# Performance work log

Hardware: AMD Instinct MI355X
Metric: run time of the kernel (lower is better)

## Reference

```python
import jax, jax.numpy as jnp
import numpy as np

N_HEAD, N_KV, HEAD_DIM, GATE_CH = 16, 4, 128, 32

def _rope(x, cos, sin):
    d = x.shape[3] // 2
    x1, x2 = x[..., :d], x[..., d:]
    return jnp.concatenate([x1 * cos + x2 * sin, x1 * (-sin) + x2 * cos], axis=3)

def _rmsnorm(x):
    xf = x.astype(jnp.float32)
    return (x * jax.lax.rsqrt(jnp.mean(xf * xf, axis=-1, keepdims=True) + 1e-6)).astype(x.dtype)

def setup_inputs() -> dict:
    key = jax.random.key(0)
    ks = jax.random.split(key, 9)
    B, T, C = 2, 2048, 2048
    return {
        "x":  jax.random.normal(ks[0], (B, T, C), jnp.float32),
        "ve": jax.random.normal(ks[1], (B, T, N_KV * HEAD_DIM), jnp.float32),
        "cos": jax.random.uniform(ks[2], (T, 1, HEAD_DIM // 2), jnp.float32),
        "sin": jax.random.uniform(ks[3], (T, 1, HEAD_DIM // 2), jnp.float32),
        "Wq": jax.random.normal(ks[4], (C, N_HEAD * HEAD_DIM), jnp.float32) * 0.02,
        "Wk": jax.random.normal(ks[5], (C, N_KV * HEAD_DIM), jnp.float32) * 0.02,
        "Wv": jax.random.normal(ks[6], (C, N_KV * HEAD_DIM), jnp.float32) * 0.02,
        "Wg": jax.random.normal(ks[7], (GATE_CH, N_KV), jnp.float32) * 0.02,
        "Wo": jax.random.normal(ks[8], (C, C), jnp.float32) * 0.02,
        "window": 1024,
    }

def reference(x, ve, cos, sin, Wq, Wk, Wv, Wg, Wo, window):
    B, T, C = x.shape
    q = (x @ Wq).reshape(B, T, N_HEAD, HEAD_DIM)
    k = (x @ Wk).reshape(B, T, N_KV, HEAD_DIM)
    v = (x @ Wv).reshape(B, T, N_KV, HEAD_DIM)
    # value-embedding gate (ve_gate active for this layer)
    gate = 2.0 * jax.nn.sigmoid(x[..., :GATE_CH] @ Wg)  # (B,T,N_KV)
    v = v + gate[..., None] * ve.reshape(B, T, N_KV, HEAD_DIM)
    q, k = _rope(q, cos, sin), _rope(k, cos, sin)
    q, k = _rmsnorm(q), _rmsnorm(k)
    # GQA: repeat kv heads (repeat_interleave over head dim)
    groups = N_HEAD // N_KV
    k = jnp.repeat(k, groups, axis=2)
    v = jnp.repeat(v, groups, axis=2)
    scale = 1.0 / np.sqrt(HEAD_DIM)
    scores = jnp.einsum("bthd,bshd->bhts", q, k) * scale  # (B,H,T,T)
    idx = jnp.arange(T)
    diff = idx[None, :] - idx[:, None]  # diff[i,j] = j - i, as in torch code
    mask = (diff >= 0) & (diff < window)
    scores = jnp.where(mask[None, None], scores, -jnp.inf)
    p = jax.nn.softmax(scores, axis=-1)
    y = jnp.einsum("bhts,bshd->bthd", p, v).reshape(B, T, C)
    return y @ Wo
```

## Files before the change

kernel.cpp:

```cpp
#include <hip/hip_runtime.h>
#include <hip/hip_bf16.h>
#include <cstdint>

typedef __hip_bfloat16 bf16;
typedef __attribute__((ext_vector_type(8))) short short8;
typedef __attribute__((ext_vector_type(4))) short short4v;
typedef __attribute__((ext_vector_type(4))) float f32x4;

#define T_   2048
#define CDIM 2048
#define NH   16
#define NKV  4
#define HD   128
#define QSCALE (0.08838834764831845f * 1.44269504088896340f)

__device__ __forceinline__ void gload_lds16(const void* g, void* l) {
  __builtin_amdgcn_global_load_lds(
      (const __attribute__((address_space(1))) void*)g,
      (__attribute__((address_space(3))) void*)l, 16, 0, 0);
}

template <int G> __device__ __forceinline__ void vm_gate() {
  if constexpr (G == 6)      asm volatile("s_waitcnt vmcnt(6)" ::: "memory");
  else if constexpr (G == 5) asm volatile("s_waitcnt vmcnt(5)" ::: "memory");
  else                       asm volatile("s_waitcnt vmcnt(0)" ::: "memory");
}

__global__ __launch_bounds__(256) void cast_x_kernel(const float4* __restrict__ in,
                                                     ushort4* __restrict__ out, int n4) {
  int i = blockIdx.x * 256 + threadIdx.x;
  if (i >= n4) return;
  float4 v = in[i];
  union { bf16 h[4]; ushort4 u; } cv;
  cv.h[0] = __float2bfloat16(v.x);
  cv.h[1] = __float2bfloat16(v.y);
  cv.h[2] = __float2bfloat16(v.z);
  cv.h[3] = __float2bfloat16(v.w);
  out[i] = cv.u;
}

__global__ __launch_bounds__(256) void cast_transpose(const float* __restrict__ W,
                                                      bf16* __restrict__ WT,
                                                      int K, int N) {
  __shared__ float tile[32][33];
  int k0 = blockIdx.y * 32, n0 = blockIdx.x * 32;
  int r = threadIdx.x >> 5, c = threadIdx.x & 31;
  for (int i = 0; i < 4; ++i)
    tile[r + i * 8][c] = W[(size_t)(k0 + r + i * 8) * N + n0 + c];
  __syncthreads();
  for (int i = 0; i < 4; ++i)
    WT[(size_t)(n0 + r + i * 8) * K + k0 + c] = __float2bfloat16(tile[c][r + i * 8]);
}

template <int MREP, int NREP, typename CT>
__global__ __launch_bounds__(512, 2) void gemm_pp(const bf16* __restrict__ A,
                                                  const bf16* __restrict__ BT,
                                                  CT* __restrict__ C,
                                                  int N, int K, int RY, int RX) {
  constexpr int BM = MREP * 32;
  constexpr int BN = NREP * 64;
  constexpr int QN = (MREP == 8) ? 4 : 2;
  constexpr int MI = MREP / 4;
  constexpr int GATE = NREP + QN - 1;
  __shared__ __align__(16) bf16 sA[2][BM * 64];
  __shared__ __align__(16) bf16 sB[2][BN * 64];

  int tid = threadIdx.x;
  int lane = tid & 63, w = tid >> 6;
  int wm = w >> 2, wn = w & 3;
  int lr = lane & 15, lk = lane >> 4;

  int xcd = blockIdx.x & 7, t = blockIdx.x >> 3;
  int by = (xcd >> 1) * RY + t / RX;
  int bx = (xcd & 1) * RX + t % RX;
  int m0 = by * BM, n0 = bx * BN;

  f32x4 acc[MREP][NREP];
#pragma unroll
  for (int m = 0; m < MREP; ++m)
#pragma unroll
    for (int n = 0; n < NREP; ++n) acc[m][n] = (f32x4){0.f, 0.f, 0.f, 0.f};

  const bf16* Abase = A + (size_t)m0 * K;
  const bf16* Bbase = BT + (size_t)n0 * K;

  auto stageB = [&](int p, int kt) {
    int kb = kt << 6;
#pragma unroll
    for (int i = 0; i < NREP; ++i) {
      int c = i * 512 + tid;
      int r = c >> 3, sl = c & 7;
      gload_lds16(Bbase + (size_t)r * K + kb + ((sl ^ (r & 7)) << 3),
                  (char*)(&sB[p][0]) + c * 16);
    }
  };
  auto stageAq = [&](int p, int kt, int q) {
    int kb = kt << 6;
    int rbase = 32 * q + ((w & 3) << 3) + ((w >> 2) * (BM / 2));
    int r = rbase + (lane >> 3), sl = lane & 7;
    gload_lds16(Abase + (size_t)r * K + kb + ((sl ^ (r & 7)) << 3),
                (char*)(&sA[p][0]) + rbase * 128 + lane * 16);
  };

  int nk = K >> 6;
  stageB(0, 0);
#pragma unroll
  for (int q = 0; q < QN; ++q) stageAq(0, 0, q);
  stageB(1, 1);
#pragma unroll
  for (int q = 0; q < QN - 1; ++q) stageAq(1, 1, q);
  vm_gate<GATE>();
  __builtin_amdgcn_s_barrier();

#define READ_A_FRAGS(PH)                                                   \
  {                                                                        \
    _Pragma("unroll")                                                      \
    for (int mi = 0; mi < MI; ++mi) {                                      \
      int row = wm * (MREP * 16) + ((PH) * MI + mi) * 16 + lr;             \
      const char* rb = sAb + row * 128;                                    \
      int rx = (row & 7) << 4;                                             \
      af[mi][0] = *(const short8*)(rb + ((lk * 16) ^ rx));                 \
      af[mi][1] = *(const short8*)(rb + ((64 + lk * 16) ^ rx));            \
    }                                                                      \
  }
#define MFMA_PH(PH)                                                        \
  __builtin_amdgcn_s_setprio(1);                                           \
  _Pragma("unroll")                                                        \
  for (int kk = 0; kk < 2; ++kk)                                           \
    _Pragma("unroll")                                                      \
    for (int mi = 0; mi < MI; ++mi)                                        \
      _Pragma("unroll")                                                    \
      for (int n = 0; n < NREP; ++n)                                       \
        acc[(PH) * MI + mi][n] = __builtin_amdgcn_mfma_f32_16x16x32_bf16(  \
            af[mi][kk], bfr[n][kk], acc[(PH) * MI + mi][n], 0, 0, 0);      \
  __builtin_amdgcn_s_setprio(0);
#define LGKM_FENCE                                                         \
  asm volatile("s_waitcnt lgkmcnt(0)" ::: "memory");                       \
  __builtin_amdgcn_sched_barrier(0);

  for (int kt = 0; kt < nk; ++kt) {
    int p = kt & 1;
    const char* sAb = (const char*)(&sA[p][0]);
    const char* sBb = (const char*)(&sB[p][0]);
    short8 bfr[NREP][2], af[MI][2];

#pragma unroll
    for (int n = 0; n < NREP; ++n) {
      int row = wn * (NREP * 16) + n * 16 + lr;
      const char* rb = sBb + row * 128;
      int rx = (row & 7) << 4;
      bfr[n][0] = *(const short8*)(rb + ((lk * 16) ^ rx));
      bfr[n][1] = *(const short8*)(rb + ((64 + lk * 16) ^ rx));
    }
    READ_A_FRAGS(0);
    if (kt + 1 < nk) stageAq(p ^ 1, kt + 1, QN - 1);
    LGKM_FENCE;
    MFMA_PH(0);
    __builtin_amdgcn_s_barrier();

    READ_A_FRAGS(1);
    if (kt + 2 < nk) {
      stageB(p, kt + 2);
      if constexpr (QN == 4) stageAq(p, kt + 2, 0);
    }
    LGKM_FENCE;
    MFMA_PH(1);
    __builtin_amdgcn_s_barrier();

    READ_A_FRAGS(2);
    if (kt + 2 < nk) stageAq(p, kt + 2, (QN == 4) ? 1 : 0);
    LGKM_FENCE;
    MFMA_PH(2);
    __builtin_amdgcn_s_barrier();

    READ_A_FRAGS(3);
    if constexpr (QN == 4) {
      if (kt + 2 < nk) stageAq(p, kt + 2, 2);
    }
    LGKM_FENCE;
    MFMA_PH(3);
    if (kt + 2 < nk) vm_gate<GATE>();
    else             vm_gate<0>();
    __builtin_amdgcn_s_barrier();
  }
#undef READ_A_FRAGS
#undef MFMA_PH
#undef LGKM_FENCE

#pragma unroll
  for (int m = 0; m < MREP; ++m)
#pragma unroll
    for (int n = 0; n < NREP; ++n)
#pragma unroll
      for (int jj = 0; jj < 4; ++jj) {
        size_t idx = (size_t)(m0 + wm * (MREP * 16) + m * 16 + lk * 4 + jj) * N +
                     n0 + wn * (NREP * 16) + n * 16 + lr;
        if constexpr (__is_same(CT, float))
          C[idx] = acc[m][n][jj];
        else
          C[idx] = __float2bfloat16(acc[m][n][jj]);
      }
}

__global__ __launch_bounds__(256) void epilogue_kernel(
    const bf16* __restrict__ qkv, const float* __restrict__ x,
    const float* __restrict__ ve, const float* __restrict__ cosT,
    const float* __restrict__ sinT, const float* __restrict__ Wg,
    bf16* __restrict__ qn, bf16* __restrict__ kn, bf16* __restrict__ vT) {
  int row = blockIdx.x;
  int bi = row >> 11, t = row & 2047;
  int tid = threadIdx.x, lane = tid & 63, w = tid >> 6;
  __shared__ float gate[NKV];
  size_t rb = (size_t)row * 3072;

  if (tid < 128) {
    int g = tid >> 5, i = tid & 31;
    float p = x[(size_t)row * CDIM + i] * Wg[i * 4 + g];
    p += __shfl_xor(p, 1);  p += __shfl_xor(p, 2);
    p += __shfl_xor(p, 4);  p += __shfl_xor(p, 8);
    p += __shfl_xor(p, 16);
    if (i == 0) gate[g] = 2.f / (1.f + __expf(-p));
  }
  __syncthreads();

  float cv = cosT[t * 64 + lane];
  float sv = sinT[t * 64 + lane];

  for (int it = 0; it < 4; ++it) {
    int h = it * 4 + w;
    float x1 = __bfloat162float(qkv[rb + h * 128 + lane]);
    float x2 = __bfloat162float(qkv[rb + h * 128 + 64 + lane]);
    float y1 = x1 * cv + x2 * sv;
    float y2 = x2 * cv - x1 * sv;
    float ss = y1 * y1 + y2 * y2;
    ss += __shfl_xor(ss, 1);  ss += __shfl_xor(ss, 2);  ss += __shfl_xor(ss, 4);
    ss += __shfl_xor(ss, 8);  ss += __shfl_xor(ss, 16); ss += __shfl_xor(ss, 32);
    float r = rsqrtf(ss * (1.f / 128.f) + 1e-6f) * QSCALE;
    size_t ob = (size_t)row * (NH * HD) + h * 128;
    qn[ob + lane] = __float2bfloat16(y1 * r);
    qn[ob + 64 + lane] = __float2bfloat16(y2 * r);
  }
  {
    int h = w;
    float x1 = __bfloat162float(qkv[rb + 2048 + h * 128 + lane]);
    float x2 = __bfloat162float(qkv[rb + 2048 + h * 128 + 64 + lane]);
    float y1 = x1 * cv + x2 * sv;
    float y2 = x2 * cv - x1 * sv;
    float ss = y1 * y1 + y2 * y2;
    ss += __shfl_xor(ss, 1);  ss += __shfl_xor(ss, 2);  ss += __shfl_xor(ss, 4);
    ss += __shfl_xor(ss, 8);  ss += __shfl_xor(ss, 16); ss += __shfl_xor(ss, 32);
    float r = rsqrtf(ss * (1.f / 128.f) + 1e-6f);
    size_t ob = (size_t)row * (NKV * HD) + h * 128;
    kn[ob + lane] = __float2bfloat16(y1 * r);
    kn[ob + 64 + lane] = __float2bfloat16(y2 * r);
  }
  for (int e = tid; e < 512; e += 256) {
    int kv = e >> 7, d = e & 127;
    float val = __bfloat162float(qkv[rb + 2560 + e]) + gate[kv] * ve[(size_t)row * 512 + e];
    vT[((size_t)(bi * NKV + kv) * HD + d) * T_ + t] = __float2bfloat16(val);
  }
}

__global__ __launch_bounds__(256, 2) void attn_kernel(
    const bf16* __restrict__ qn, const bf16* __restrict__ kn,
    const bf16* __restrict__ vT, bf16* __restrict__ y,
    const int* __restrict__ winp) {
  __shared__ __align__(16) bf16 sK[2][64 * 128];
  __shared__ __align__(16) bf16 sV[2][128 * 64];

  int win = *winp;
  int id = blockIdx.x;
  int g  = id & 7;
  int bi = g >> 2, kvh = g & 3;
  int rem = id >> 3;
  int h  = kvh * 4 + (rem & 3);
  int q0 = (rem >> 2) << 7;
  int tid = threadIdx.x;
  int lane = tid & 63, w = tid >> 6;
  int lr = lane & 15, lk = lane >> 4;

  short8 qfA[4], qfB[4];
  {
    const bf16* qrA = qn + (size_t)(bi * T_ + q0 + w * 32 + lr) * (NH * HD) + h * HD;
    const bf16* qrB = qrA + (size_t)16 * (NH * HD);
#pragma unroll
    for (int c = 0; c < 4; ++c) {
      qfA[c] = *(const short8*)(qrA + c * 32 + lk * 8);
      qfB[c] = *(const short8*)(qrB + c * 32 + lk * 8);
    }
  }

  int kge[4], klb[4], vge[4], vlbA[4], vlbB[4];
#pragma unroll
  for (int i = 0; i < 4; ++i) {
    int c = i * 256 + tid;
    int kr = c >> 4, ks = c & 15;
    kge[i] = kr * (NKV * HD) + ks * 8;
    klb[i] = kr * 256 + ((ks ^ (kr & 7)) << 4);
    int vr = c >> 3, vs = c & 7;
    vge[i] = vr * T_ + vs * 8;
    int hh = vs >> 2, m = vs & 3, a = m >> 1;
    int sA = 8 * ((2 * m) & 3) + 4 * a;
    int sB = 8 * ((2 * m + 1) & 3) + 4 * a;
    int tA = 64 * hh + 2 * sA, tB = 64 * hh + 2 * sB;
    vlbA[i] = vr * 128 + (((tA >> 4) ^ (vr & 7)) << 4) + (tA & 15);
    vlbB[i] = vr * 128 + (((tB >> 4) ^ (vr & 7)) << 4) + (tB & 15);
  }
  const bf16* kpane = kn + (size_t)bi * T_ * (NKV * HD) + kvh * HD;
  const bf16* vpane = vT + (size_t)(bi * NKV + kvh) * HD * T_;

  short8 kreg[4], vreg[4];
  auto LOAD = [&](int jtx) {
    const bf16* kb = kpane + (size_t)(jtx << 6) * (NKV * HD);
    const bf16* vb = vpane + (jtx << 6);
#pragma unroll
    for (int i = 0; i < 4; ++i) kreg[i] = *(const short8*)(kb + kge[i]);
#pragma unroll
    for (int i = 0; i < 4; ++i) vreg[i] = *(const short8*)(vb + vge[i]);
  };
  auto WRITE = [&](int b) {
    char* kBuf = (char*)(&sK[b][0]);
    char* vBuf = (char*)(&sV[b][0]);
#pragma unroll
    for (int i = 0; i < 4; ++i) *(short8*)(kBuf + klb[i]) = kreg[i];
#pragma unroll
    for (int i = 0; i < 4; ++i) {
      union { short8 s8; short4v s4[2]; } u;
      u.s8 = vreg[i];
      *(short4v*)(vBuf + vlbA[i]) = u.s4[0];
      *(short4v*)(vBuf + vlbB[i]) = u.s4[1];
    }
  };

  f32x4 o0[8], o1[8];
#pragma unroll
  for (int i = 0; i < 8; ++i) {
    o0[i] = (f32x4){0.f, 0.f, 0.f, 0.f};
    o1[i] = (f32x4){0.f, 0.f, 0.f, 0.f};
  }
  float lp0 = 0.f, lp1 = 0.f;

  int jt0 = q0 >> 6;
  int hi = q0 + 126 + win; if (hi > T_ - 1) hi = T_ - 1;
  int jt1 = hi >> 6;

  LOAD(jt0);
  WRITE(0);
  if (jt0 < jt1) LOAD(jt0 + 1);
  asm volatile("s_waitcnt lgkmcnt(0)\n\ts_barrier" ::: "memory");

  int irow0 = q0 + w * 32 + lr;
  int klo = lk * 4;

  int p = 0;
  for (int jt = jt0; jt <= jt1; ++jt) {
    int j0 = jt << 6;

    if (jt < jt1) {
      WRITE(p ^ 1);
      if (jt + 1 < jt1) LOAD(jt + 2);
    }

    const char* sKb = (const char*)(&sK[p][0]);
    const char* sVb = (const char*)(&sV[p][0]);

    f32x4 s0[4], s1[4];
#pragma unroll
    for (int sub = 0; sub < 4; ++sub) {
      s0[sub] = (f32x4){0.f, 0.f, 0.f, 0.f};
      s1[sub] = (f32x4){0.f, 0.f, 0.f, 0.f};
    }
    __builtin_amdgcn_s_setprio(1);
#pragma unroll
    for (int sub = 0; sub < 4; ++sub) {
      int kr = sub * 16 + lr;
      int rx = (kr & 7) << 4;
      const char* rowb = sKb + kr * 256;
#pragma unroll
      for (int c = 0; c < 4; ++c) {
        short8 kf = *(const short8*)(rowb + ((c * 64 + lk * 16) ^ rx));
        s0[sub] = __builtin_amdgcn_mfma_f32_16x16x32_bf16(kf, qfA[c], s0[sub], 0, 0, 0);
        s1[sub] = __builtin_amdgcn_mfma_f32_16x16x32_bf16(kf, qfB[c], s1[sub], 0, 0, 0);
      }
    }
    __builtin_amdgcn_s_setprio(0);

    bool full = (j0 >= q0 + 128) && (j0 + 64 <= q0 + win);
    int koff0 = j0 - irow0;
    int koff1 = koff0 - 16;

    short8 pA0, pA1, pB0, pB1;
    {
      unsigned pk[8];
#pragma unroll
      for (int sub = 0; sub < 4; ++sub) {
        float p0 = exp2f(s0[sub][0]), p1 = exp2f(s0[sub][1]);
        float p2 = exp2f(s0[sub][2]), p3 = exp2f(s0[sub][3]);
        if (!full) {
          int base = koff0 + sub * 16 + klo;
          p0 = ((unsigned)(base + 0) < (unsigned)win) ? p0 : 0.f;
          p1 = ((unsigned)(base + 1) < (unsigned)win) ? p1 : 0.f;
          p2 = ((unsigned)(base + 2) < (unsigned)win) ? p2 : 0.f;
          p3 = ((unsigned)(base + 3) < (unsigned)win) ? p3 : 0.f;
        }
        lp0 += (p0 + p1) + (p2 + p3);
        asm("v_cvt_pk_bf16_f32 %0, %1, %2" : "=v"(pk[sub * 2])     : "v"(p0), "v"(p1));
        asm("v_cvt_pk_bf16_f32 %0, %1, %2" : "=v"(pk[sub * 2 + 1]) : "v"(p2), "v"(p3));
      }
      union { unsigned u[4]; short8 s8; } c0, c1;
      c0.u[0] = pk[0]; c0.u[1] = pk[1]; c0.u[2] = pk[2]; c0.u[3] = pk[3];
      c1.u[0] = pk[4]; c1.u[1] = pk[5]; c1.u[2] = pk[6]; c1.u[3] = pk[7];
      pA0 = c0.s8; pA1 = c1.s8;
    }
    {
      unsigned pk[8];
#pragma unroll
      for (int sub = 0; sub < 4; ++sub) {
        float p0 = exp2f(s1[sub][0]), p1 = exp2f(s1[sub][1]);
        float p2 = exp2f(s1[sub][2]), p3 = exp2f(s1[sub][3]);
        if (!full) {
          int base = koff1 + sub * 16 + klo;
          p0 = ((unsigned)(base + 0) < (unsigned)win) ? p0 : 0.f;
          p1 = ((unsigned)(base + 1) < (unsigned)win) ? p1 : 0.f;
          p2 = ((unsigned)(base + 2) < (unsigned)win) ? p2 : 0.f;
          p3 = ((unsigned)(base + 3) < (unsigned)win) ? p3 : 0.f;
        }
        lp1 += (p0 + p1) + (p2 + p3);
        asm("v_cvt_pk_bf16_f32 %0, %1, %2" : "=v"(pk[sub * 2])     : "v"(p0), "v"(p1));
        asm("v_cvt_pk_bf16_f32 %0, %1, %2" : "=v"(pk[sub * 2 + 1]) : "v"(p2), "v"(p3));
      }
      union { unsigned u[4]; short8 s8; } c0, c1;
      c0.u[0] = pk[0]; c0.u[1] = pk[1]; c0.u[2] = pk[2]; c0.u[3] = pk[3];
      c1.u[0] = pk[4]; c1.u[1] = pk[5]; c1.u[2] = pk[6]; c1.u[3] = pk[7];
      pB0 = c0.s8; pB1 = c1.s8;
    }

    __builtin_amdgcn_s_setprio(1);
#pragma unroll
    for (int nb = 0; nb < 8; ++nb) {
      int vr = nb * 16 + lr;
      int vrx = (vr & 7) << 4;
      const char* vb = sVb + vr * 128;
      short8 vf0 = *(const short8*)(vb + ((lk * 16) ^ vrx));
      short8 vf1 = *(const short8*)(vb + ((64 + lk * 16) ^ vrx));
      o0[nb] = __builtin_amdgcn_mfma_f32_16x16x32_bf16(pA0, vf0, o0[nb], 0, 0, 0);
      o0[nb] = __builtin_amdgcn_mfma_f32_16x16x32_bf16(pA1, vf1, o0[nb], 0, 0, 0);
      o1[nb] = __builtin_amdgcn_mfma_f32_16x16x32_bf16(pB0, vf0, o1[nb], 0, 0, 0);
      o1[nb] = __builtin_amdgcn_mfma_f32_16x16x32_bf16(pB1, vf1, o1[nb], 0, 0, 0);
    }
    __builtin_amdgcn_s_setprio(0);

    asm volatile("s_waitcnt lgkmcnt(0)\n\ts_barrier" ::: "memory");
    p ^= 1;
  }

  float l0 = lp0, l1 = lp1;
  l0 += __shfl_xor(l0, 16); l0 += __shfl_xor(l0, 32);
  l1 += __shfl_xor(l1, 16); l1 += __shfl_xor(l1, 32);
#pragma unroll
  for (int jj = 0; jj < 4; ++jj) {
    float inv0 = 1.f / __shfl(l0, klo + jj);
    float inv1 = 1.f / __shfl(l1, klo + jj);
    size_t ob0 = (size_t)(bi * T_ + q0 + w * 32 + klo + jj) * (NH * HD) + h * HD;
    size_t ob1 = ob0 + (size_t)16 * (NH * HD);
#pragma unroll
    for (int nb = 0; nb < 8; ++nb) {
      y[ob0 + nb * 16 + lr] = __float2bfloat16(o0[nb][jj] * inv0);
      y[ob1 + nb * 16 + lr] = __float2bfloat16(o1[nb][jj] * inv1);
    }
  }
}

extern "C" void kernel_launch(void* const* d_in, const int* in_sizes, int n_in,
                              void* d_out, int out_size, void* d_ws, size_t ws_size,
                              hipStream_t stream) {
  const float* x    = (const float*)d_in[0];
  const float* ve   = (const float*)d_in[1];
  const float* cosT = (const float*)d_in[2];
  const float* sinT = (const float*)d_in[3];
  const float* Wq   = (const float*)d_in[4];
  const float* Wk   = (const float*)d_in[5];
  const float* Wv   = (const float*)d_in[6];
  const float* Wg   = (const float*)d_in[7];
  const float* Wo   = (const float*)d_in[8];
  const int*   win  = (const int*)d_in[9];
  float* out = (float*)d_out;

  char* ws = (char*)d_ws;
  bf16*  xb   = (bf16*)(ws);
  bf16*  wT   = (bf16*)(ws + 16777216);
  bf16*  woT  = (bf16*)(ws + 29360128);
  bf16*  qkvb = (bf16*)(ws + 37748736);
  bf16*  qn   = (bf16*)(ws + 62914560);
  bf16*  kn   = (bf16*)(ws + 79691776);
  bf16*  vTb  = (bf16*)(ws + 83886080);
  bf16*  y    = qkvb;

  cast_x_kernel<<<8192, 256, 0, stream>>>((const float4*)x, (ushort4*)xb, 2097152);
  cast_transpose<<<dim3(64, 64), 256, 0, stream>>>(Wq, wT, 2048, 2048);
  cast_transpose<<<dim3(16, 64), 256, 0, stream>>>(Wk, wT + (size_t)2048 * 2048, 2048, 512);
  cast_transpose<<<dim3(16, 64), 256, 0, stream>>>(Wv, wT + (size_t)2560 * 2048, 2048, 512);
  cast_transpose<<<dim3(64, 64), 256, 0, stream>>>(Wo, woT, 2048, 2048);

  gemm_pp<8, 3, bf16><<<256, 512, 0, stream>>>(xb, wT, qkvb, 3072, 2048, 4, 8);
  epilogue_kernel<<<4096, 256, 0, stream>>>(qkvb, x, ve, cosT, sinT, Wg, qn, kn, vTb);
  attn_kernel<<<512, 256, 0, stream>>>(qn, kn, vTb, y, win);
  gemm_pp<4, 4, float><<<256, 512, 0, stream>>>(y, woT, out, 2048, 2048, 8, 4);
}
```

Baseline: 193.4 us.

## Use 256x256-tile ping-pong GEMM with half-tile staged loads for QKV projection

```diff
diff --git a/kernel.cpp b/kernel.cpp
--- a/kernel.cpp
+++ b/kernel.cpp
@@ -23,6 +23,7 @@
 template <int G> __device__ __forceinline__ void vm_gate() {
   if constexpr (G == 6)      asm volatile("s_waitcnt vmcnt(6)" ::: "memory");
   else if constexpr (G == 5) asm volatile("s_waitcnt vmcnt(5)" ::: "memory");
+  else if constexpr (G == 4) asm volatile("s_waitcnt vmcnt(4)" ::: "memory");
   else                       asm volatile("s_waitcnt vmcnt(0)" ::: "memory");
 }
 
@@ -50,6 +51,146 @@
   __syncthreads();
   for (int i = 0; i < 4; ++i)
     WT[(size_t)(n0 + r + i * 8) * K + k0 + c] = __float2bfloat16(tile[c][r + i * 8]);
+}
+
+__global__ __launch_bounds__(512, 2) void gemm_m201(const bf16* __restrict__ A,
+                                                    const bf16* __restrict__ BT,
+                                                    bf16* __restrict__ C,
+                                                    int N, int K, int RY, int RX) {
+  __shared__ __align__(16) bf16 sA[2][256 * 64];
+  __shared__ __align__(16) bf16 sB[2][256 * 64];
+
+  int tid = threadIdx.x;
+  int lane = tid & 63, w = tid >> 6;
+  int wm = w >> 2, wn = w & 3;
+  int lr = lane & 15, lk = lane >> 4;
+
+  int xcd = blockIdx.x & 7, t = blockIdx.x >> 3;
+  int by = (xcd >> 1) * RY + t / RX;
+  int bx = (xcd & 1) * RX + t % RX;
+  int m0 = by * 256, n0 = bx * 256;
+
+  f32x4 acc[8][4];
+#pragma unroll
+  for (int m = 0; m < 8; ++m)
+#pragma unroll
+    for (int n = 0; n < 4; ++n) acc[m][n] = (f32x4){0.f, 0.f, 0.f, 0.f};
+
+  const bf16* Abase = A + (size_t)m0 * K;
+  const bf16* Bbase = BT + (size_t)n0 * K;
+
+  auto stA = [&](int p, int kt, int h) {
+    int kb = kt << 6;
+#pragma unroll
+    for (int i = 0; i < 2; ++i) {
+      int c = i * 512 + tid;
+      int r = (c >> 3) + h * 128, sl = c & 7;
+      gload_lds16(Abase + (size_t)r * K + kb + ((sl ^ (r & 7)) << 3),
+                  (char*)(&sA[p][0]) + r * 128 + sl * 16);
+    }
+  };
+  auto stB = [&](int p, int kt, int h) {
+    int kb = kt << 6;
+#pragma unroll
+    for (int i = 0; i < 2; ++i) {
+      int c = i * 512 + tid;
+      int r = (c >> 3) + h * 128, sl = c & 7;
+      gload_lds16(Bbase + (size_t)r * K + kb + ((sl ^ (r & 7)) << 3),
+                  (char*)(&sB[p][0]) + r * 128 + sl * 16);
+    }
+  };
+
+  int nk = K >> 6;
+  stB(0, 0, 0); stB(0, 0, 1); stA(0, 0, 0); stA(0, 0, 1);
+  stB(1, 1, 0); stA(1, 1, 0);
+  vm_gate<4>();
+  __builtin_amdgcn_s_barrier();
+
+#define READ_AF(QM)                                                        \
+  {                                                                        \
+    _Pragma("unroll")                                                      \
+    for (int m = 0; m < 4; ++m) {                                          \
+      int row = wm * 128 + (QM) * 64 + m * 16 + lr;                        \
+      const char* rb = sAb + row * 128;                                    \
+      int rx = (row & 7) << 4;                                             \
+      af[m][0] = *(const short8*)(rb + ((lk * 16) ^ rx));                  \
+      af[m][1] = *(const short8*)(rb + ((64 + lk * 16) ^ rx));             \
+    }                                                                      \
+  }
+#define READ_BF(DST, QN)                                                   \
+  {                                                                        \
+    _Pragma("unroll")                                                      \
+    for (int n = 0; n < 2; ++n) {                                          \
+      int row = wn * 64 + (QN) * 32 + n * 16 + lr;                         \
+      const char* rb = sBb + row * 128;                                    \
+      int rx = (row & 7) << 4;                                             \
+      DST[n][0] = *(const short8*)(rb + ((lk * 16) ^ rx));                 \
+      DST[n][1] = *(const short8*)(rb + ((64 + lk * 16) ^ rx));            \
+    }                                                                      \
+  }
+#define MFMA_QUAD(BF, QM, QN)                                              \
+  __builtin_amdgcn_s_setprio(1);                                           \
+  _Pragma("unroll")                                                        \
+  for (int kk = 0; kk < 2; ++kk)                                           \
+    _Pragma("unroll")                                                      \
+    for (int m = 0; m < 4; ++m)                                            \
+      _Pragma("unroll")                                                    \
+      for (int n = 0; n < 2; ++n)                                          \
+        acc[(QM) * 4 + m][(QN) * 2 + n] =                                  \
+            __builtin_amdgcn_mfma_f32_16x16x32_bf16(                       \
+                af[m][kk], BF[n][kk], acc[(QM) * 4 + m][(QN) * 2 + n],     \
+                0, 0, 0);                                                  \
+  __builtin_amdgcn_s_setprio(0);
+#define PH_SYNC                                                            \
+  __builtin_amdgcn_s_barrier();                                            \
+  asm volatile("s_waitcnt lgkmcnt(0)" ::: "memory");                       \
+  __builtin_amdgcn_sched_barrier(0);
+
+  for (int kt = 0; kt < nk; ++kt) {
+    int p = kt & 1;
+    const char* sAb = (const char*)(&sA[p][0]);
+    const char* sBb = (const char*)(&sB[p][0]);
+    short8 af[4][2], bfr0[2][2], bfr1[2][2];
+
+    READ_AF(0);
+    READ_BF(bfr0, 0);
+    if (kt + 1 < nk) stB(p ^ 1, kt + 1, 1);
+    PH_SYNC;
+    MFMA_QUAD(bfr0, 0, 0);
+    __builtin_amdgcn_s_barrier();
+
+    READ_BF(bfr1, 1);
+    if (kt + 1 < nk) stA(p ^ 1, kt + 1, 1);
+    PH_SYNC;
+    MFMA_QUAD(bfr1, 0, 1);
+    __builtin_amdgcn_s_barrier();
+
+    READ_AF(1);
+    if (kt + 2 < nk) stB(p, kt + 2, 0);
+    PH_SYNC;
+    MFMA_QUAD(bfr1, 1, 1);
+    __builtin_amdgcn_s_barrier();
+
+    if (kt + 2 < nk) stA(p, kt + 2, 0);
+    PH_SYNC;
+    MFMA_QUAD(bfr0, 1, 0);
+    if (kt + 2 < nk) vm_gate<4>();
+    else             vm_gate<0>();
+    __builtin_amdgcn_s_barrier();
+  }
+#undef READ_AF
+#undef READ_BF
+#undef MFMA_QUAD
+#undef PH_SYNC
+
+#pragma unroll
+  for (int m = 0; m < 8; ++m)
+#pragma unroll
+    for (int n = 0; n < 4; ++n)
+#pragma unroll
+      for (int jj = 0; jj < 4; ++jj)
+        C[(size_t)(m0 + wm * 128 + m * 16 + lk * 4 + jj) * N +
+          n0 + wn * 64 + n * 16 + lr] = __float2bfloat16(acc[m][n][jj]);
 }
 
 template <int MREP, int NREP, typename CT>
@@ -431,7 +572,7 @@
       }
       union { unsigned u[4]; short8 s8; } c0, c1;
       c0.u[0] = pk[0]; c0.u[1] = pk[1]; c0.u[2] = pk[2]; c0.u[3] = pk[3];
-      c1.u[0] = pk[4]; c1.u[1] = pk[5]; c1.u[2] = pk[6]; c1.u[3] = pk[7];
+      c1.u[0] = pk[4]; c1.u[1] = pk[5]; c1.u[2] = pk[6]; c1.u[7 - 4] = pk[7];
       pB0 = c0.s8; pB1 = c1.s8;
     }
 
@@ -502,7 +643,7 @@
   cast_transpose<<<dim3(16, 64), 256, 0, stream>>>(Wv, wT + (size_t)2560 * 2048, 2048, 512);
   cast_transpose<<<dim3(64, 64), 256, 0, stream>>>(Wo, woT, 2048, 2048);
 
-  gemm_pp<8, 3, bf16><<<256, 512, 0, stream>>>(xb, wT, qkvb, 3072, 2048, 4, 8);
+  gemm_m201<<<192, 512, 0, stream>>>(xb, wT, qkvb, 3072, 2048, 4, 6);
   epilogue_kernel<<<4096, 256, 0, stream>>>(qkvb, x, ve, cosT, sinT, Wg, qn, kn, vTb);
   attn_kernel<<<512, 256, 0, stream>>>(qn, kn, vTb, y, win);
   gemm_pp<4, 4, float><<<256, 512, 0, stream>>>(y, woT, out, 2048, 2048, 8, 4);
```

New measurement: 197.1 us. No clear change (+1.9%).
